# Optimization experiments

Hardware: AMD Instinct MI355X
Metric: run time of the kernel (lower is better)

Reference implementation:

```python
import jax, jax.numpy as jnp
import numpy as np

B, S, HID = 1, 2048, 4096
NH, NKV, HD = 32, 8, 128
INIT, RECENT, HEAVY = 128, 512, 512
THETA = 10000.0


def _rope(x, pos):
    # x: [B,H,S,D]; standard Llama rotary embedding (rotate_half convention)
    d = x.shape[-1]
    inv = 1.0 / (THETA ** (jnp.arange(0, d, 2, dtype=jnp.float32) / d))
    ang = pos[:, None] * inv[None, :]                      # [S, D/2]
    cos = jnp.concatenate([jnp.cos(ang), jnp.cos(ang)], -1)  # [S, D]
    sin = jnp.concatenate([jnp.sin(ang), jnp.sin(ang)], -1)
    x1, x2 = x[..., : d // 2], x[..., d // 2:]
    rot = jnp.concatenate([-x2, x1], -1)
    return x * cos + rot * sin


def setup_inputs() -> dict:
    key = jax.random.key(0)
    ks = jax.random.split(key, 5)
    s = 1.0 / np.sqrt(HID)
    return {
        "hidden_states": jax.random.normal(ks[0], (B, S, HID), jnp.float32),
        "wq": jax.random.normal(ks[1], (HID, NH * HD), jnp.float32) * s,
        "wk": jax.random.normal(ks[2], (HID, NKV * HD), jnp.float32) * s,
        "wv": jax.random.normal(ks[3], (HID, NKV * HD), jnp.float32) * s,
        "wo": jax.random.normal(ks[4], (NH * HD, HID), jnp.float32) * s,
    }


def reference(hidden_states, wq, wk, wv, wo):
    # QKV projections (no bias, per attention_bias=False)
    q = (hidden_states @ wq).reshape(B, S, NH, HD).transpose(0, 2, 1, 3)   # [B,NH,S,D]
    k = (hidden_states @ wk).reshape(B, S, NKV, HD).transpose(0, 2, 1, 3)  # [B,NKV,S,D]
    v = (hidden_states @ wv).reshape(B, S, NKV, HD).transpose(0, 2, 1, 3)
    pos = jnp.arange(S, dtype=jnp.float32)
    q = _rope(q, pos)
    k = _rope(k, pos)
    # repeat_kv for GQA
    rep = NH // NKV
    k = jnp.repeat(k, rep, axis=1)
    v = jnp.repeat(v, rep, axis=1)

    scores = jnp.einsum('bhqd,bhkd->bhqk', q, k) / np.sqrt(HD)  # [B,NH,S,S]

    qi = jnp.arange(S)[:, None]
    ki = jnp.arange(S)[None, :]
    causal = ki <= qi
    # causal_heavy_recent_mask: tril(diag = k - q - recent) with [:, :init] = False
    middle = (ki <= qi - RECENT) & (ki >= INIT)   # heavy-hitter eligible region
    base = causal & jnp.logical_not(middle)       # init + recent tokens always kept

    neg = jnp.finfo(scores.dtype).min
    mid_scores = jnp.where(middle[None, None], scores, neg)
    _, idx = jax.lax.top_k(mid_scores, HEAVY)     # [B,NH,S,HEAVY]
    flat = idx.reshape(-1, HEAVY)
    rows = jnp.arange(flat.shape[0])[:, None]
    heavy = jnp.zeros((flat.shape[0], S), dtype=bool).at[rows, flat].set(True)
    heavy = heavy.reshape(B, NH, S, S) & middle[None, None]

    mask = base[None, None] | heavy
    attn = jax.nn.softmax(jnp.where(mask, scores, neg), axis=-1)
    out = jnp.einsum('bhqk,bhkd->bhqd', attn, v)
    out = out.transpose(0, 2, 1, 3).reshape(B, S, NH * HD)
    return out @ wo
```

## Files before the change

### kernel.cpp

```cpp
#include <hip/hip_runtime.h>
#include <math.h>

#define S_LEN 2048
#define HID_N 4096
#define NH 32
#define NKV 8
#define HD 128
#define INIT_N 128
#define RECENT_N 512
#define HEAVY_N 512
#define SCALE_QK 0.08838834764831845f

typedef __attribute__((ext_vector_type(8))) short short8;
typedef __attribute__((ext_vector_type(4))) float float4v;

__device__ __forceinline__ unsigned short f2bf(float f) {
  unsigned u = __float_as_uint(f);
  unsigned r = (u + 0x7FFFu + ((u >> 16) & 1u)) >> 16;
  return (unsigned short)r;
}

__device__ __forceinline__ float bf2f(unsigned u) { return __uint_as_float(u << 16); }

__device__ __forceinline__ unsigned fkey16(unsigned u) {
  return (u & 0x8000u) ? ((~u) & 0xFFFFu) : (u | 0x8000u);
}

__device__ __forceinline__ void gld_lds16(const unsigned short* g, unsigned short* l) {
  __builtin_amdgcn_global_load_lds(
      (const __attribute__((address_space(1))) unsigned int*)g,
      (__attribute__((address_space(3))) unsigned int*)l, 16, 0, 0);
}

#define VMCNT(n) asm volatile("s_waitcnt vmcnt(" #n ")" ::: "memory")

__global__ __launch_bounds__(256) void cast_bf16x8(const float* __restrict__ x,
                                                   unsigned short* __restrict__ y, int n) {
  int i = (blockIdx.x * 256 + threadIdx.x) << 3;
  if (i >= n) return;
  float4 a = *(const float4*)(x + i);
  float4 b = *(const float4*)(x + i + 4);
  union { unsigned short u[8]; short8 v; } o;
  o.u[0] = f2bf(a.x); o.u[1] = f2bf(a.y); o.u[2] = f2bf(a.z); o.u[3] = f2bf(a.w);
  o.u[4] = f2bf(b.x); o.u[5] = f2bf(b.y); o.u[6] = f2bf(b.z); o.u[7] = f2bf(b.w);
  *(short8*)(y + i) = o.v;
}

__global__ __launch_bounds__(256) void transpose_cast(const float* __restrict__ w,
                                                      unsigned short* __restrict__ wt,
                                                      int R, int C, int ldw) {
  __shared__ unsigned short t[64][65];
  const int c0 = blockIdx.x * 64;
  const int r0 = blockIdx.y * 64;
  const int tx = threadIdx.x & 63;
  const int ty = threadIdx.x >> 6;
#pragma unroll
  for (int i = 0; i < 16; ++i)
    t[ty + 4 * i][tx] = f2bf(w[(size_t)(r0 + ty + 4 * i) * ldw + c0 + tx]);
  __syncthreads();
#pragma unroll
  for (int i = 0; i < 16; ++i)
    wt[(size_t)(c0 + ty + 4 * i) * R + r0 + tx] = t[tx][ty + 4 * i];
}

__global__ __launch_bounds__(512, 2)
void gemm256(const unsigned short* __restrict__ A,
             const unsigned short* __restrict__ BT,
             float* __restrict__ C, int M, int N, int K) {
  __shared__ __align__(16) unsigned short lds[65536];
  const int tid = threadIdx.x;
  const int lane = tid & 63;
  const int wid = tid >> 6;
  const int wr = wid >> 2;
  const int wc = wid & 3;
  const int col = lane & 15;
  const int quad = lane >> 4;

  const int gx = gridDim.x;
  const int nwg = gx * gridDim.y;
  int lin = blockIdx.y * gx + blockIdx.x;
  lin = (lin & 7) * (nwg >> 3) + (lin >> 3);
  const int m0 = (lin / gx) << 8;
  const int n0 = (lin % gx) << 8;
  const int NT = K >> 6;

  const int sdst = wid << 9;
  const int grow = tid >> 3;
  const int gcol = (tid & 7) << 3;

#define STG2(G, B0_, LOFF, RB0, RB1, KC)                                      \
  do {                                                                        \
    gld_lds16(G + (size_t)((B0_) + (RB0) + grow) * K + (KC) + gcol,           \
              &lds[(LOFF) + (RB0) * 64 + sdst]);                              \
    gld_lds16(G + (size_t)((B0_) + (RB1) + grow) * K + (KC) + gcol,           \
              &lds[(LOFF) + (RB1) * 64 + sdst]);                              \
  } while (0)

  float4v acc[8][4] = {};

  STG2(BT, n0, 32768, 0, 64, 0);
  STG2(BT, n0, 32768, 128, 192, 0);
  STG2(A, m0, 0, 0, 128, 0);
  STG2(A, m0, 0, 64, 192, 0);
  if (NT > 1) {
    STG2(BT, n0, 32768 + 16384, 0, 64, 64);
    STG2(BT, n0, 32768 + 16384, 128, 192, 64);
    STG2(A, m0, 16384, 0, 128, 64);
    VMCNT(8);
  } else {
    VMCNT(2);
  }
  __builtin_amdgcn_s_barrier();

#pragma unroll 1
  for (int t = 0; t < NT; ++t) {
    const int cb = (t & 1) << 14;
    const int nb = cb ^ 16384;
    const int cbB = 32768 + cb;
    const int kc1 = (t + 1) << 6;
    const int kc2 = (t + 2) << 6;
    const bool h1 = (t + 1) < NT;
    const bool h2 = (t + 2) < NT;
    const int abase = cb + (wr * 128 + col) * 64 + (quad << 3);

    short8 b8[4][2];
#pragma unroll
    for (int ni = 0; ni < 4; ++ni)
#pragma unroll
      for (int kk = 0; kk < 2; ++kk)
        b8[ni][kk] = *(const short8*)&lds[cbB + (wc * 64 + ni * 16 + col) * 64 +
                                          (quad << 3) + kk * 32];
    {
      short8 x0 = *(const short8*)&lds[abase + 0 * 64];
      short8 x1 = *(const short8*)&lds[abase + 0 * 64 + 32];
      short8 x2 = *(const short8*)&lds[abase + 16 * 64];
      short8 x3 = *(const short8*)&lds[abase + 16 * 64 + 32];
      if (h1) STG2(A, m0, nb, 64, 192, kc1);
      __builtin_amdgcn_s_barrier();
      asm volatile("s_waitcnt lgkmcnt(0)" ::: "memory");
      __builtin_amdgcn_sched_barrier(0);
      __builtin_amdgcn_s_setprio(1);
#pragma unroll
      for (int ni = 0; ni < 4; ++ni) {
        acc[0][ni] = __builtin_amdgcn_mfma_f32_16x16x32_bf16(x0, b8[ni][0], acc[0][ni], 0, 0, 0);
        acc[0][ni] = __builtin_amdgcn_mfma_f32_16x16x32_bf16(x1, b8[ni][1], acc[0][ni], 0, 0, 0);
        acc[1][ni] = __builtin_amdgcn_mfma_f32_16x16x32_bf16(x2, b8[ni][0], acc[1][ni], 0, 0, 0);
        acc[1][ni] = __builtin_amdgcn_mfma_f32_16x16x32_bf16(x3, b8[ni][1], acc[1][ni], 0, 0, 0);
      }
      __builtin_amdgcn_s_setprio(0);
      __builtin_amdgcn_s_barrier();
    }
    {
      short8 x0 = *(const short8*)&lds[abase + 32 * 64];
      short8 x1 = *(const short8*)&lds[abase + 32 * 64 + 32];
      short8 x2 = *(const short8*)&lds[abase + 48 * 64];
      short8 x3 = *(const short8*)&lds[abase + 48 * 64 + 32];
      if (h2) STG2(BT, n0, cbB, 0, 64, kc2);
      if (h2) { VMCNT(10); } else if (h1) { VMCNT(8); } else { VMCNT(0); }
      __builtin_amdgcn_s_barrier();
      asm volatile("s_waitcnt lgkmcnt(0)" ::: "memory");
      __builtin_amdgcn_sched_barrier(0);
      __builtin_amdgcn_s_setprio(1);
#pragma unroll
      for (int ni = 0; ni < 4; ++ni) {
        acc[2][ni] = __builtin_amdgcn_mfma_f32_16x16x32_bf16(x0, b8[ni][0], acc[2][ni], 0, 0, 0);
        acc[2][ni] = __builtin_amdgcn_mfma_f32_16x16x32_bf16(x1, b8[ni][1], acc[2][ni], 0, 0, 0);
        acc[3][ni] = __builtin_amdgcn_mfma_f32_16x16x32_bf16(x2, b8[ni][0], acc[3][ni], 0, 0, 0);
        acc[3][ni] = __builtin_amdgcn_mfma_f32_16x16x32_bf16(x3, b8[ni][1], acc[3][ni], 0, 0, 0);
      }
      __builtin_amdgcn_s_setprio(0);
      __builtin_amdgcn_s_barrier();
    }
    {
      short8 x0 = *(const short8*)&lds[abase + 64 * 64];
      short8 x1 = *(const short8*)&lds[abase + 64 * 64 + 32];
      short8 x2 = *(const short8*)&lds[abase + 80 * 64];
      short8 x3 = *(const short8*)&lds[abase + 80 * 64 + 32];
      if (h2) STG2(BT, n0, cbB, 128, 192, kc2);
      __builtin_amdgcn_s_barrier();
      asm volatile("s_waitcnt lgkmcnt(0)" ::: "memory");
      __builtin_amdgcn_sched_barrier(0);
      __builtin_amdgcn_s_setprio(1);
#pragma unroll
      for (int ni = 0; ni < 4; ++ni) {
        acc[4][ni] = __builtin_amdgcn_mfma_f32_16x16x32_bf16(x0, b8[ni][0], acc[4][ni], 0, 0, 0);
        acc[4][ni] = __builtin_amdgcn_mfma_f32_16x16x32_bf16(x1, b8[ni][1], acc[4][ni], 0, 0, 0);
        acc[5][ni] = __builtin_amdgcn_mfma_f32_16x16x32_bf16(x2, b8[ni][0], acc[5][ni], 0, 0, 0);
        acc[5][ni] = __builtin_amdgcn_mfma_f32_16x16x32_bf16(x3, b8[ni][1], acc[5][ni], 0, 0, 0);
      }
      __builtin_amdgcn_s_setprio(0);
      __builtin_amdgcn_s_barrier();
    }
    {
      short8 x0 = *(const short8*)&lds[abase + 96 * 64];
      short8 x1 = *(const short8*)&lds[abase + 96 * 64 + 32];
      short8 x2 = *(const short8*)&lds[abase + 112 * 64];
      short8 x3 = *(const short8*)&lds[abase + 112 * 64 + 32];
      if (h2) STG2(A, m0, cb, 0, 128, kc2);
      if (h2) { VMCNT(8); } else if (h1) { VMCNT(2); }
      __builtin_amdgcn_s_barrier();
      asm volatile("s_waitcnt lgkmcnt(0)" ::: "memory");
      __builtin_amdgcn_sched_barrier(0);
      __builtin_amdgcn_s_setprio(1);
#pragma unroll
      for (int ni = 0; ni < 4; ++ni) {
        acc[6][ni] = __builtin_amdgcn_mfma_f32_16x16x32_bf16(x0, b8[ni][0], acc[6][ni], 0, 0, 0);
        acc[6][ni] = __builtin_amdgcn_mfma_f32_16x16x32_bf16(x1, b8[ni][1], acc[6][ni], 0, 0, 0);
        acc[7][ni] = __builtin_amdgcn_mfma_f32_16x16x32_bf16(x2, b8[ni][0], acc[7][ni], 0, 0, 0);
        acc[7][ni] = __builtin_amdgcn_mfma_f32_16x16x32_bf16(x3, b8[ni][1], acc[7][ni], 0, 0, 0);
      }
      __builtin_amdgcn_s_setprio(0);
      __builtin_amdgcn_s_barrier();
    }
  }

#pragma unroll
  for (int mi = 0; mi < 8; ++mi)
#pragma unroll
    for (int ni = 0; ni < 4; ++ni) {
      size_t base = (size_t)(m0 + wr * 128 + mi * 16 + (quad << 2)) * N +
                    n0 + wc * 64 + ni * 16 + col;
      C[base] = acc[mi][ni][0];
      C[base + N] = acc[mi][ni][1];
      C[base + 2 * (size_t)N] = acc[mi][ni][2];
      C[base + 3 * (size_t)N] = acc[mi][ni][3];
    }
#undef STG2
}

__global__ __launch_bounds__(256) void rope_cast(const float* __restrict__ x,
                                                 unsigned short* __restrict__ y,
                                                 int nheads, int ldx, int ldy) {
  int idx = blockIdx.x * 256 + threadIdx.x;
  int i = idx & 63;
  int rest = idx >> 6;
  int hh = rest % nheads;
  int s = rest / nheads;
  if (s >= S_LEN) return;
  const float* p = x + (size_t)s * ldx + hh * HD;
  unsigned short* o = y + (size_t)s * ldy + hh * HD;
  float inv = (float)(1.0 / pow(10000.0, (double)(2 * i) / 128.0));
  float ang = (float)s * inv;
  float c = cosf(ang);
  float sn = sinf(ang);
  float x1 = p[i];
  float x2 = p[i + 64];
  o[i] = f2bf(x1 * c - x2 * sn);
  o[i + 64] = f2bf(x2 * c + x1 * sn);
}

template <int SMAX>
__global__ __launch_bounds__(512, 4)
void attn_mfma(const unsigned short* __restrict__ qb,
               const unsigned short* __restrict__ kb,
               const unsigned short* __restrict__ vt,
               unsigned short* __restrict__ ao16, int qbase) {
  const int qi0 = (qbase + blockIdx.x) << 4;
  const int h = blockIdx.y;
  const int g = h >> 2;
  const int tid = threadIdx.x;
  const int lane = tid & 63;
  const int wid = tid >> 6;
  const int col = lane & 15;
  const int quad = lane >> 4;
  const int nkm = qi0 + 16;
  const int nkm32 = (nkm + 31) & ~31;

  __shared__ __align__(16) unsigned short sc[16 * SMAX];
  __shared__ float sumv[16];

  short8 qf[4];
  {
    const unsigned short* qrow = qb + (size_t)(qi0 + col) * (NH * HD) + h * HD + (quad << 3);
#pragma unroll
    for (int dt = 0; dt < 4; ++dt) qf[dt] = *(const short8*)(qrow + dt * 32);
  }
  const int ntiles = nkm >> 4;
  int t = wid;
  for (; t + 8 < ntiles; t += 16) {
    const int k0a = t << 4;
    const int k0b = (t + 8) << 4;
    const unsigned short* kra = kb + (size_t)(k0a + col) * (NKV * HD) + g * HD + (quad << 3);
    const unsigned short* krb = kb + (size_t)(k0b + col) * (NKV * HD) + g * HD + (quad << 3);
    short8 kfa[4], kfb[4];
#pragma unroll
    for (int dt = 0; dt < 4; ++dt) kfa[dt] = *(const short8*)(kra + dt * 32);
#pragma unroll
    for (int dt = 0; dt < 4; ++dt) kfb[dt] = *(const short8*)(krb + dt * 32);
    float4v acca = {}, accb = {};
#pragma unroll
    for (int dt = 0; dt < 4; ++dt) {
      acca = __builtin_amdgcn_mfma_f32_16x16x32_bf16(qf[dt], kfa[dt], acca, 0, 0, 0);
      accb = __builtin_amdgcn_mfma_f32_16x16x32_bf16(qf[dt], kfb[dt], accb, 0, 0, 0);
    }
#pragma unroll
    for (int r = 0; r < 4; ++r) {
      int q = (quad << 2) + r;
      sc[(q * SMAX + k0a + col) ^ ((q & 7) << 3)] = f2bf(acca[r] * SCALE_QK);
      sc[(q * SMAX + k0b + col) ^ ((q & 7) << 3)] = f2bf(accb[r] * SCALE_QK);
    }
  }
  if (t < ntiles) {
    const int k0 = t << 4;
    const unsigned short* krow = kb + (size_t)(k0 + col) * (NKV * HD) + g * HD + (quad << 3);
    float4v acc = {};
#pragma unroll
    for (int dt = 0; dt < 4; ++dt) {
      short8 kf = *(const short8*)(krow + dt * 32);
      acc = __builtin_amdgcn_mfma_f32_16x16x32_bf16(qf[dt], kf, acc, 0, 0, 0);
    }
#pragma unroll
    for (int r = 0; r < 4; ++r) {
      int q = (quad << 2) + r;
      sc[(q * SMAX + k0 + col) ^ ((q & 7) << 3)] = f2bf(acc[r] * SCALE_QK);
    }
  }
  __syncthreads();

  const unsigned long long lmlt = (1ull << lane) - 1ull;
#pragma unroll 1
  for (int rr = 0; rr < 2; ++rr) {
    const int r = (wid << 1) + rr;
    const int qi = qi0 + r;
    const int mhi = qi - RECENT_N;
    const int m = mhi - INIT_N + 1;
    const bool need = (SMAX > 1024) && (m > HEAVY_N);
    const unsigned swz = (r & 7) << 3;
    const int rbase = r * SMAX;

    unsigned T = 0, rem = 0;
    if (need) {
      unsigned myk[22];
#pragma unroll
      for (int j = 0; j < 11; ++j) {
        int off = (lane + (j << 6)) << 1;
        unsigned u = *(const unsigned*)&sc[(rbase + INIT_N + off) ^ swz];
        unsigned f0 = fkey16(u & 0xFFFFu);
        unsigned f1 = fkey16(u >> 16);
        myk[2 * j] = (off < m) ? f0 : 0u;
        myk[2 * j + 1] = (off + 1 < m) ? f1 : 0u;
      }
      unsigned prefix = 0, rm = HEAVY_N;
#pragma unroll 1
      for (int bit = 15; bit >= 0; --bit) {
        unsigned target = (prefix >> bit) | 1u;
        unsigned cnt = 0;
#pragma unroll
        for (int j = 0; j < 22; ++j)
          cnt += (unsigned)__popcll(__ballot((myk[j] >> bit) == target));
        if (cnt >= rm) prefix |= (1u << bit);
        else rm -= cnt;
      }
      T = prefix;
      rem = rm;
    }

    float mx = -3.402823466e38f;
#pragma unroll 1
    for (int c0 = 0; c0 <= qi; c0 += 128) {
      int k2 = c0 + (lane << 1);
      unsigned u = *(const unsigned*)&sc[(rbase + k2) ^ swz];
      float s0 = bf2f(u & 0xFFFFu);
      float s1 = bf2f(u >> 16);
      if (k2 <= qi) mx = fmaxf(mx, s0);
      if (k2 + 1 <= qi) mx = fmaxf(mx, s1);
    }
#pragma unroll
    for (int off = 32; off; off >>= 1) mx = fmaxf(mx, __shfl_xor(mx, off, 64));

    float sum = 0.f;
    unsigned cum = 0;
#pragma unroll 1
    for (int c0 = 0; c0 < nkm32; c0 += 128) {
      int k2 = c0 + (lane << 1);
      int idx = (rbase + k2) ^ swz;
      unsigned u = *(const unsigned*)&sc[idx];
      bool ic0 = k2 <= qi, ic1 = (k2 + 1) <= qi;
      bool sel0, sel1;
      if (!need) {
        sel0 = ic0;
        sel1 = ic1;
      } else {
        bool mid0 = ic0 && (k2 >= INIT_N) && (k2 <= mhi);
        bool mid1 = ic1 && (k2 + 1 >= INIT_N) && (k2 + 1 <= mhi);
        unsigned f0 = fkey16(u & 0xFFFFu);
        unsigned f1 = fkey16(u >> 16);
        unsigned long long eq0 = __ballot(mid0 && (f0 == T));
        unsigned long long eq1 = __ballot(mid1 && (f1 == T));
        unsigned pre0 = cum + (unsigned)__popcll(eq0 & lmlt) + (unsigned)__popcll(eq1 & lmlt);
        unsigned pre1 = pre0 + (unsigned)((eq0 >> lane) & 1ull);
        sel0 = ic0 && (!mid0 || (f0 > T) || ((f0 == T) && (pre0 < rem)));
        sel1 = ic1 && (!mid1 || (f1 > T) || ((f1 == T) && (pre1 < rem)));
        cum += (unsigned)__popcll(eq0) + (unsigned)__popcll(eq1);
      }
      float e0 = sel0 ? __expf(bf2f(u & 0xFFFFu) - mx) : 0.f;
      float e1 = sel1 ? __expf(bf2f(u >> 16) - mx) : 0.f;
      sum += e0 + e1;
      *(unsigned*)&sc[idx] = (unsigned)f2bf(e0) | ((unsigned)f2bf(e1) << 16);
    }
#pragma unroll
    for (int off = 32; off; off >>= 1) sum += __shfl_xor(sum, off, 64);
    if (lane == 0) sumv[r] = sum;
  }
  __syncthreads();

  float4v a0 = {}, b0 = {};
  const int db = wid << 4;
  const unsigned short* vrow = vt + (size_t)(g * HD + db + col) * S_LEN + (quad << 3);
  const unsigned pswz = (unsigned)((col & 7) << 3);
  int k0 = 0;
  for (; k0 + 32 < nkm32; k0 += 64) {
    short8 pf0 = *(const short8*)&sc[(col * SMAX + k0 + (quad << 3)) ^ pswz];
    short8 pf1 = *(const short8*)&sc[(col * SMAX + k0 + 32 + (quad << 3)) ^ pswz];
    short8 v0 = *(const short8*)(vrow + k0);
    short8 v1 = *(const short8*)(vrow + k0 + 32);
    a0 = __builtin_amdgcn_mfma_f32_16x16x32_bf16(pf0, v0, a0, 0, 0, 0);
    b0 = __builtin_amdgcn_mfma_f32_16x16x32_bf16(pf1, v1, b0, 0, 0, 0);
  }
  if (k0 < nkm32) {
    short8 pf = *(const short8*)&sc[(col * SMAX + k0 + (quad << 3)) ^ pswz];
    short8 v0 = *(const short8*)(vrow + k0);
    a0 = __builtin_amdgcn_mfma_f32_16x16x32_bf16(pf, v0, a0, 0, 0, 0);
  }
  a0 += b0;
#pragma unroll
  for (int r = 0; r < 4; ++r) {
    int qq = (quad << 2) + r;
    float inv = 1.0f / sumv[qq];
    size_t o = (size_t)(qi0 + qq) * (NH * HD) + h * HD + db;
    ao16[o + col] = f2bf(a0[r] * inv);
  }
}

extern "C" void kernel_launch(void* const* d_in, const int* in_sizes, int n_in,
                              void* d_out, int out_size, void* d_ws, size_t ws_size,
                              hipStream_t stream) {
  const float* hidden = (const float*)d_in[0];
  const float* wq = (const float*)d_in[1];
  const float* wk = (const float*)d_in[2];
  const float* wv = (const float*)d_in[3];
  const float* wo = (const float*)d_in[4];
  float* out = (float*)d_out;

  float* ws = (float*)d_ws;
  const size_t M1 = 1024 * 1024;
  float* qkv = ws;
  unsigned short* qb16 = (unsigned short*)(ws + 12 * M1);
  unsigned short* hb = (unsigned short*)(ws + 16 * M1);
  unsigned short* aob = hb;
  unsigned short* wqkvT = (unsigned short*)(ws + 20 * M1);
  unsigned short* woT = wqkvT;
  unsigned short* kb16 = (unsigned short*)(ws + 28 * M1);
  unsigned short* vT16 = (unsigned short*)(ws + 29 * M1);

  dim3 blk(256);
  const int NE = S_LEN * HID_N;

  cast_bf16x8<<<NE / 2048, blk, 0, stream>>>(hidden, hb, NE);
  transpose_cast<<<dim3(HID_N / 64, HID_N / 64), blk, 0, stream>>>(wq, wqkvT, HID_N, HID_N, HID_N);
  transpose_cast<<<dim3((NKV * HD) / 64, HID_N / 64), blk, 0, stream>>>(
      wk, wqkvT + (size_t)HID_N * HID_N, HID_N, NKV * HD, NKV * HD);
  transpose_cast<<<dim3((NKV * HD) / 64, HID_N / 64), blk, 0, stream>>>(
      wv, wqkvT + (size_t)(HID_N + NKV * HD) * HID_N, HID_N, NKV * HD, NKV * HD);

  gemm256<<<dim3(6144 / 256, S_LEN / 256), dim3(512), 0, stream>>>(hb, wqkvT, qkv, S_LEN, 6144, HID_N);

  transpose_cast<<<dim3(HID_N / 64, HID_N / 64), blk, 0, stream>>>(wo, woT, NH * HD, HID_N, HID_N);

  rope_cast<<<(S_LEN * NH * 64) / 256, blk, 0, stream>>>(qkv, qb16, NH, 6144, NH * HD);
  rope_cast<<<(S_LEN * NKV * 64) / 256, blk, 0, stream>>>(qkv + HID_N, kb16, NKV, 6144, NKV * HD);
  transpose_cast<<<dim3((NKV * HD) / 64, S_LEN / 64), blk, 0, stream>>>(
      qkv + HID_N + NKV * HD, vT16, S_LEN, NKV * HD, 6144);

  attn_mfma<2048><<<dim3(64, NH), dim3(512), 0, stream>>>(qb16, kb16, vT16, aob, 64);
  attn_mfma<1024><<<dim3(64, NH), dim3(512), 0, stream>>>(qb16, kb16, vT16, aob, 0);

  gemm256<<<dim3(HID_N / 256, S_LEN / 256), dim3(512), 0, stream>>>(aob, woT, out, S_LEN, HID_N, NH * HD);
}
```

Baseline: 909.2 us.

## Swizzle GEMM LDS layout and split-K the output projection across two slices

XORs the K-column offset within each LDS row by the row index, for both the global-to-LDS stores and the fragment reads, to avoid LDS bank conflicts in the bf16 MFMA GEMM. The output projection GEMM is split along K into two halves via blockIdx.z, doubling the grid from 128 to 256 workgroups for better CU occupancy. A second partial buffer is written to workspace and summed by an extra elementwise add kernel, which adds memory traffic and a launch.

```diff
diff --git a/kernel.cpp b/kernel.cpp
--- a/kernel.cpp
+++ b/kernel.cpp
@@ -46,6 +46,16 @@
   *(short8*)(y + i) = o.v;
 }
 
+__global__ __launch_bounds__(256) void add_f32x4(float* __restrict__ y,
+                                                 const float* __restrict__ x, int n) {
+  int i = (blockIdx.x * 256 + threadIdx.x) << 2;
+  if (i >= n) return;
+  float4 a = *(const float4*)(y + i);
+  float4 b = *(const float4*)(x + i);
+  a.x += b.x; a.y += b.y; a.z += b.z; a.w += b.w;
+  *(float4*)(y + i) = a;
+}
+
 __global__ __launch_bounds__(256) void transpose_cast(const float* __restrict__ w,
                                                       unsigned short* __restrict__ wt,
                                                       int R, int C, int ldw) {
@@ -66,7 +76,8 @@
 __global__ __launch_bounds__(512, 2)
 void gemm256(const unsigned short* __restrict__ A,
              const unsigned short* __restrict__ BT,
-             float* __restrict__ C, int M, int N, int K) {
+             float* __restrict__ C0, float* __restrict__ C1,
+             int M, int N, int KT, int lda, int ldb) {
   __shared__ __align__(16) unsigned short lds[65536];
   const int tid = threadIdx.x;
   const int lane = tid & 63;
@@ -76,36 +87,42 @@
   const int col = lane & 15;
   const int quad = lane >> 4;
 
+  A += (size_t)blockIdx.z * KT;
+  BT += (size_t)blockIdx.z * KT;
+  float* __restrict__ C = blockIdx.z ? C1 : C0;
+
   const int gx = gridDim.x;
   const int nwg = gx * gridDim.y;
   int lin = blockIdx.y * gx + blockIdx.x;
   lin = (lin & 7) * (nwg >> 3) + (lin >> 3);
   const int m0 = (lin / gx) << 8;
   const int n0 = (lin % gx) << 8;
-  const int NT = K >> 6;
+  const int NT = KT >> 6;
 
   const int sdst = wid << 9;
   const int grow = tid >> 3;
-  const int gcol = (tid & 7) << 3;
-
-#define STG2(G, B0_, LOFF, RB0, RB1, KC)                                      \
+  const int gcolsw = ((tid & 7) << 3) ^ (((tid >> 3) & 7) << 3);
+  const int o0 = ((quad << 3) ^ ((col & 7) << 3));
+  const int o1 = o0 ^ 32;
+
+#define STG2(G, LD, GB, LOFF, RB0, RB1, KC)                                   \
   do {                                                                        \
-    gld_lds16(G + (size_t)((B0_) + (RB0) + grow) * K + (KC) + gcol,           \
+    gld_lds16(G + (size_t)((GB) + (RB0) + grow) * (LD) + (KC) + gcolsw,       \
               &lds[(LOFF) + (RB0) * 64 + sdst]);                              \
-    gld_lds16(G + (size_t)((B0_) + (RB1) + grow) * K + (KC) + gcol,           \
+    gld_lds16(G + (size_t)((GB) + (RB1) + grow) * (LD) + (KC) + gcolsw,       \
               &lds[(LOFF) + (RB1) * 64 + sdst]);                              \
   } while (0)
 
   float4v acc[8][4] = {};
 
-  STG2(BT, n0, 32768, 0, 64, 0);
-  STG2(BT, n0, 32768, 128, 192, 0);
-  STG2(A, m0, 0, 0, 128, 0);
-  STG2(A, m0, 0, 64, 192, 0);
+  STG2(BT, ldb, n0, 32768, 0, 64, 0);
+  STG2(BT, ldb, n0, 32768, 128, 192, 0);
+  STG2(A, lda, m0, 0, 0, 128, 0);
+  STG2(A, lda, m0, 0, 64, 192, 0);
   if (NT > 1) {
-    STG2(BT, n0, 32768 + 16384, 0, 64, 64);
-    STG2(BT, n0, 32768 + 16384, 128, 192, 64);
-    STG2(A, m0, 16384, 0, 128, 64);
+    STG2(BT, ldb, n0, 32768 + 16384, 0, 64, 64);
+    STG2(BT, ldb, n0, 32768 + 16384, 128, 192, 64);
+    STG2(A, lda, m0, 16384, 0, 128, 64);
     VMCNT(8);
   } else {
     VMCNT(2);
@@ -121,21 +138,21 @@
     const int kc2 = (t + 2) << 6;
     const bool h1 = (t + 1) < NT;
     const bool h2 = (t + 2) < NT;
-    const int abase = cb + (wr * 128 + col) * 64 + (quad << 3);
+    const int abase = cb + (wr * 128 + col) * 64;
 
     short8 b8[4][2];
 #pragma unroll
-    for (int ni = 0; ni < 4; ++ni)
-#pragma unroll
-      for (int kk = 0; kk < 2; ++kk)
-        b8[ni][kk] = *(const short8*)&lds[cbB + (wc * 64 + ni * 16 + col) * 64 +
-                                          (quad << 3) + kk * 32];
+    for (int ni = 0; ni < 4; ++ni) {
+      const int bb = cbB + (wc * 64 + ni * 16 + col) * 64;
+      b8[ni][0] = *(const short8*)&lds[bb + o0];
+      b8[ni][1] = *(const short8*)&lds[bb + o1];
+    }
     {
-      short8 x0 = *(const short8*)&lds[abase + 0 * 64];
-      short8 x1 = *(const short8*)&lds[abase + 0 * 64 + 32];
-      short8 x2 = *(const short8*)&lds[abase + 16 * 64];
-      short8 x3 = *(const short8*)&lds[abase + 16 * 64 + 32];
-      if (h1) STG2(A, m0, nb, 64, 192, kc1);
+      short8 x0 = *(const short8*)&lds[abase + 0 * 64 + o0];
+      short8 x1 = *(const short8*)&lds[abase + 0 * 64 + o1];
+      short8 x2 = *(const short8*)&lds[abase + 16 * 64 + o0];
+      short8 x3 = *(const short8*)&lds[abase + 16 * 64 + o1];
+      if (h1) STG2(A, lda, m0, nb, 64, 192, kc1);
       __builtin_amdgcn_s_barrier();
       asm volatile("s_waitcnt lgkmcnt(0)" ::: "memory");
       __builtin_amdgcn_sched_barrier(0);
@@ -151,11 +168,11 @@
       __builtin_amdgcn_s_barrier();
     }
     {
-      short8 x0 = *(const short8*)&lds[abase + 32 * 64];
-      short8 x1 = *(const short8*)&lds[abase + 32 * 64 + 32];
-      short8 x2 = *(const short8*)&lds[abase + 48 * 64];
-      short8 x3 = *(const short8*)&lds[abase + 48 * 64 + 32];
-      if (h2) STG2(BT, n0, cbB, 0, 64, kc2);
+      short8 x0 = *(const short8*)&lds[abase + 32 * 64 + o0];
+      short8 x1 = *(const short8*)&lds[abase + 32 * 64 + o1];
+      short8 x2 = *(const short8*)&lds[abase + 48 * 64 + o0];
+      short8 x3 = *(const short8*)&lds[abase + 48 * 64 + o1];
+      if (h2) STG2(BT, ldb, n0, cbB, 0, 64, kc2);
       if (h2) { VMCNT(10); } else if (h1) { VMCNT(8); } else { VMCNT(0); }
       __builtin_amdgcn_s_barrier();
       asm volatile("s_waitcnt lgkmcnt(0)" ::: "memory");
@@ -172,11 +189,11 @@
       __builtin_amdgcn_s_barrier();
     }
     {
-      short8 x0 = *(const short8*)&lds[abase + 64 * 64];
-      short8 x1 = *(const short8*)&lds[abase + 64 * 64 + 32];
-      short8 x2 = *(const short8*)&lds[abase + 80 * 64];
-      short8 x3 = *(const short8*)&lds[abase + 80 * 64 + 32];
-      if (h2) STG2(BT, n0, cbB, 128, 192, kc2);
+      short8 x0 = *(const short8*)&lds[abase + 64 * 64 + o0];
+      short8 x1 = *(const short8*)&lds[abase + 64 * 64 + o1];
+      short8 x2 = *(const short8*)&lds[abase + 80 * 64 + o0];
+      short8 x3 = *(const short8*)&lds[abase + 80 * 64 + o1];
+      if (h2) STG2(BT, ldb, n0, cbB, 128, 192, kc2);
       __builtin_amdgcn_s_barrier();
       asm volatile("s_waitcnt lgkmcnt(0)" ::: "memory");
       __builtin_amdgcn_sched_barrier(0);
@@ -192,11 +209,11 @@
       __builtin_amdgcn_s_barrier();
     }
     {
-      short8 x0 = *(const short8*)&lds[abase + 96 * 64];
-      short8 x1 = *(const short8*)&lds[abase + 96 * 64 + 32];
-      short8 x2 = *(const short8*)&lds[abase + 112 * 64];
-      short8 x3 = *(const short8*)&lds[abase + 112 * 64 + 32];
-      if (h2) STG2(A, m0, cb, 0, 128, kc2);
+      short8 x0 = *(const short8*)&lds[abase + 96 * 64 + o0];
+      short8 x1 = *(const short8*)&lds[abase + 96 * 64 + o1];
+      short8 x2 = *(const short8*)&lds[abase + 112 * 64 + o0];
+      short8 x3 = *(const short8*)&lds[abase + 112 * 64 + o1];
+      if (h2) STG2(A, lda, m0, cb, 0, 128, kc2);
       if (h2) { VMCNT(8); } else if (h1) { VMCNT(2); }
       __builtin_amdgcn_s_barrier();
       asm volatile("s_waitcnt lgkmcnt(0)" ::: "memory");
@@ -445,6 +462,7 @@
   float* ws = (float*)d_ws;
   const size_t M1 = 1024 * 1024;
   float* qkv = ws;
+  float* P1 = ws;
   unsigned short* qb16 = (unsigned short*)(ws + 12 * M1);
   unsigned short* hb = (unsigned short*)(ws + 16 * M1);
   unsigned short* aob = hb;
@@ -463,7 +481,8 @@
   transpose_cast<<<dim3((NKV * HD) / 64, HID_N / 64), blk, 0, stream>>>(
       wv, wqkvT + (size_t)(HID_N + NKV * HD) * HID_N, HID_N, NKV * HD, NKV * HD);
 
-  gemm256<<<dim3(6144 / 256, S_LEN / 256), dim3(512), 0, stream>>>(hb, wqkvT, qkv, S_LEN, 6144, HID_N);
+  gemm256<<<dim3(24, 8, 1), dim3(512), 0, stream>>>(hb, wqkvT, qkv, qkv, S_LEN, 6144,
+                                                    HID_N, HID_N, HID_N);
 
   transpose_cast<<<dim3(HID_N / 64, HID_N / 64), blk, 0, stream>>>(wo, woT, NH * HD, HID_N, HID_N);
 
@@ -475,5 +494,7 @@
   attn_mfma<2048><<<dim3(64, NH), dim3(512), 0, stream>>>(qb16, kb16, vT16, aob, 64);
   attn_mfma<1024><<<dim3(64, NH), dim3(512), 0, stream>>>(qb16, kb16, vT16, aob, 0);
 
-  gemm256<<<dim3(HID_N / 256, S_LEN / 256), dim3(512), 0, stream>>>(aob, woT, out, S_LEN, HID_N, NH * HD);
-}
+  gemm256<<<dim3(16, 8, 2), dim3(512), 0, stream>>>(aob, woT, out, P1, S_LEN, HID_N,
+                                                    2048, NH * HD, HID_N);
+  add_f32x4<<<NE / 1024, blk, 0, stream>>>(out, P1, NE);
+}
```

Result: faster. 812.2 us (-10.7%).
